# Performance work log

Hardware: AMD Instinct MI355X
Metric: run time of the kernel (lower is better)

## Reference

```python
import jax, jax.numpy as jnp
import numpy as np

B, D, H, N, M, K = 128, 256, 4, 256, 256, 10  # M=256 is hardcoded in the original repeat(1,1,1,256)
DIM = D // H  # per-head dim = 64


def setup_inputs() -> dict:
    key = jax.random.key(0)
    ks = jax.random.split(key, 10)
    s = 0.05  # weight scale
    return {
        "x": jax.random.normal(ks[0], (B, D, N), jnp.float32),
        "source": jax.random.normal(ks[1], (B, D, M), jnp.float32),
        "Wq": jax.random.normal(ks[2], (D, D), jnp.float32) * s,
        "bq": jax.random.normal(ks[3], (D,), jnp.float32) * s,
        "Wk": jax.random.normal(ks[4], (D, D), jnp.float32) * s,
        "bk": jax.random.normal(ks[5], (D,), jnp.float32) * s,
        "Wv": jax.random.normal(ks[6], (D, D), jnp.float32) * s,
        "bv": jax.random.normal(ks[7], (D,), jnp.float32) * s,
        "Wm": jax.random.normal(ks[8], (D, D), jnp.float32) * s,
        "bm": jax.random.normal(ks[9], (D,), jnp.float32) * s,
        "k": K,
    }


def _pointwise(W, b, x):
    # nn.Conv1d(d, d, kernel_size=1): per-point linear over channel dim
    return jnp.einsum('ef,bfn->ben', W, x) + b[None, :, None]


def reference(x, source, Wq, bq, Wk, bk, Wv, bv, Wm, bm, k):
    b, d, n = x.shape
    # torch .view(b, dim, heads, -1) splits channels as (dim, heads)
    q = _pointwise(Wq, bq, x).reshape(b, DIM, H, n)
    kk = _pointwise(Wk, bk, source).reshape(b, DIM, H, -1)
    v = _pointwise(Wv, bv, source).reshape(b, DIM, H, -1)

    scores = jnp.einsum('bdhn,bdhm->bhnm', q, kk) / jnp.sqrt(jnp.asarray(DIM, x.dtype))
    # per-row top-k threshold: keep only scores >= k-th largest, softmax over kept
    thresh = jax.lax.top_k(scores, k)[0][..., k - 1:k]  # [b,h,n,1]
    mask = scores >= thresh
    neg = jnp.finfo(scores.dtype).min
    prob = jax.nn.softmax(jnp.where(mask, scores, neg), axis=-1)
    prob = jnp.where(mask, prob, jnp.zeros((), scores.dtype))

    out = jnp.einsum('bhnm,bdhm->bdhn', prob, v).reshape(b, d, n)
    return _pointwise(Wm, bm, out)
```

## Files before the change

### kernel.cpp

```cpp
#include <hip/hip_runtime.h>
#include <hip/hip_bf16.h>

#define BB   128
#define DDIM 256
#define HH   4
#define NNN  256
#define MMM  256

typedef __hip_bfloat16 bf16;
typedef short  short8   __attribute__((ext_vector_type(8)));
typedef unsigned short ushort8_t __attribute__((ext_vector_type(8)));
typedef float  f32x4    __attribute__((ext_vector_type(4)));

__device__ __forceinline__ unsigned short f2bf(float x) {
    unsigned u = __builtin_bit_cast(unsigned, x);
    u += 0x7FFFu + ((u >> 16) & 1u);
    return (unsigned short)(u >> 16);
}
__device__ __forceinline__ float bf2f(unsigned short b) {
    unsigned u = ((unsigned)b) << 16;
    return __builtin_bit_cast(float, u);
}

__device__ __forceinline__ void xpose4(float v[4], const int p) {
    float ta = __shfl_xor((p & 1) ? v[0] : v[1], 1, 64);
    float tb = __shfl_xor((p & 1) ? v[2] : v[3], 1, 64);
    float u0 = (p & 1) ? ta : v[0];
    float u1 = (p & 1) ? v[1] : ta;
    float u2 = (p & 1) ? tb : v[2];
    float u3 = (p & 1) ? v[3] : tb;
    float tc = __shfl_xor((p & 2) ? u0 : u2, 2, 64);
    float td = __shfl_xor((p & 2) ? u1 : u3, 2, 64);
    v[0] = (p & 2) ? tc : u0;
    v[1] = (p & 2) ? td : u1;
    v[2] = (p & 2) ? u2 : tc;
    v[3] = (p & 2) ? u3 : td;
}

__device__ __forceinline__ void split3_store8k(char* dst, const float v[4]) {
    unsigned short h[4], m[4], l[4];
    #pragma unroll
    for (int i = 0; i < 4; ++i) {
        h[i] = f2bf(v[i]);
        float r1 = v[i] - bf2f(h[i]);
        m[i] = f2bf(r1);
        float r2 = r1 - bf2f(m[i]);
        l[i] = f2bf(r2);
    }
    uint2 hp, mp, lp;
    hp.x = (unsigned)h[0] | ((unsigned)h[1] << 16);
    hp.y = (unsigned)h[2] | ((unsigned)h[3] << 16);
    mp.x = (unsigned)m[0] | ((unsigned)m[1] << 16);
    mp.y = (unsigned)m[2] | ((unsigned)m[3] << 16);
    lp.x = (unsigned)l[0] | ((unsigned)l[1] << 16);
    lp.y = (unsigned)l[2] | ((unsigned)l[3] << 16);
    *(uint2*)dst = hp;
    *(uint2*)(dst + 8192) = mp;
    *(uint2*)(dst + 16384) = lp;
}

__device__ __forceinline__ void split2_store(char* dst, const float v[4]) {
    unsigned short h[4], m[4];
    #pragma unroll
    for (int i = 0; i < 4; ++i) {
        h[i] = f2bf(v[i]);
        float r1 = v[i] - bf2f(h[i]);
        m[i] = f2bf(r1);
    }
    uint2 hp, mp;
    hp.x = (unsigned)h[0] | ((unsigned)h[1] << 16);
    hp.y = (unsigned)h[2] | ((unsigned)h[3] << 16);
    mp.x = (unsigned)m[0] | ((unsigned)m[1] << 16);
    mp.y = (unsigned)m[2] | ((unsigned)m[3] << 16);
    *(uint2*)dst = hp;
    *(uint2*)(dst + 16384) = mp;
}

__device__ __forceinline__ void ldx4(const float* p, float v[4]) {
    const float4 f = *(const float4*)p;
    v[0] = f.x; v[1] = f.y; v[2] = f.z; v[3] = f.w;
}
__device__ __forceinline__ void ldx4(const bf16* p, float v[4]) {
    uint2 u = *(const uint2*)p;
    v[0] = bf2f((unsigned short)(u.x & 0xFFFF));
    v[1] = bf2f((unsigned short)(u.x >> 16));
    v[2] = bf2f((unsigned short)(u.y & 0xFFFF));
    v[3] = bf2f((unsigned short)(u.y >> 16));
}

__device__ __forceinline__ float max16v(const float* w) {
    float a = fmaxf(fmaxf(w[0], w[1]),  fmaxf(w[2], w[3]));
    float b = fmaxf(fmaxf(w[4], w[5]),  fmaxf(w[6], w[7]));
    float c = fmaxf(fmaxf(w[8], w[9]),  fmaxf(w[10], w[11]));
    float d = fmaxf(fmaxf(w[12], w[13]), fmaxf(w[14], w[15]));
    return fmaxf(fmaxf(a, b), fmaxf(c, d));
}
__device__ __forceinline__ float gmax16(float v) {
    v = fmaxf(v, __shfl_xor(v, 1, 64));
    v = fmaxf(v, __shfl_xor(v, 2, 64));
    v = fmaxf(v, __shfl_xor(v, 4, 64));
    v = fmaxf(v, __shfl_xor(v, 8, 64));
    return v;
}
__device__ __forceinline__ float gsum16(float v) {
    v += __shfl_xor(v, 1, 64);
    v += __shfl_xor(v, 2, 64);
    v += __shfl_xor(v, 4, 64);
    v += __shfl_xor(v, 8, 64);
    return v;
}

__global__ __launch_bounds__(256)
void proj_kernel(const float* __restrict__ X, const float* __restrict__ W,
                 const float* __restrict__ bias, float* __restrict__ Y) {
    __shared__ float Wt[32][68];
    __shared__ float Xt[32][132];

    const int t  = threadIdx.x;
    const int tx = t & 31;
    const int ty = t >> 5;
    const int n0 = blockIdx.x * 128;
    const int e0 = blockIdx.y * 64;
    const int b  = blockIdx.z;
    const size_t plane = (size_t)b * DDIM * NNN;

    float acc[8][4] = {};

    for (int f0 = 0; f0 < DDIM; f0 += 32) {
        #pragma unroll
        for (int i = 0; i < 8; ++i) {
            int idx = t + i * 256;
            int fl = idx & 31, el = idx >> 5;
            Wt[fl][el] = W[(size_t)(e0 + el) * DDIM + f0 + fl];
        }
        #pragma unroll
        for (int i = 0; i < 4; ++i) {
            int idx = t + i * 256;
            int fl = idx >> 5, nl4 = idx & 31;
            *(float4*)&Xt[fl][nl4 * 4] =
                *(const float4*)&X[plane + (size_t)(f0 + fl) * NNN + n0 + nl4 * 4];
        }
        __syncthreads();

        #pragma unroll
        for (int ff = 0; ff < 32; ++ff) {
            const float4 av0 = *(const float4*)&Wt[ff][ty * 8];
            const float4 av1 = *(const float4*)&Wt[ff][ty * 8 + 4];
            const float4 bv  = *(const float4*)&Xt[ff][tx * 4];
            const float a[8] = {av0.x, av0.y, av0.z, av0.w, av1.x, av1.y, av1.z, av1.w};
            const float c[4] = {bv.x, bv.y, bv.z, bv.w};
            #pragma unroll
            for (int i2 = 0; i2 < 8; ++i2)
                #pragma unroll
                for (int j = 0; j < 4; ++j)
                    acc[i2][j] = fmaf(a[i2], c[j], acc[i2][j]);
        }
        __syncthreads();
    }

    #pragma unroll
    for (int i2 = 0; i2 < 8; ++i2) {
        const int e = e0 + ty * 8 + i2;
        const float bs = bias[e];
        const size_t off = plane + (size_t)e * NNN + n0 + tx * 4;
        float4 o;
        o.x = acc[i2][0] + bs; o.y = acc[i2][1] + bs;
        o.z = acc[i2][2] + bs; o.w = acc[i2][3] + bs;
        *(float4*)&Y[off] = o;
    }
}

template <typename TIN, typename TOUT>
__global__ __launch_bounds__(512, 2)
void projm_kernel(const TIN* __restrict__ X, const float* __restrict__ W,
                  const float* __restrict__ bias, TOUT* __restrict__ Y) {
    extern __shared__ __align__(16) char smem[];

    const int t    = threadIdx.x;
    const int lane = t & 63;
    const int w    = t >> 6;
    const int c16  = lane & 15;
    const int g    = (lane >> 4) & 3;
    const int p    = lane & 3;
    const int G    = lane >> 2;

    const int n0 = blockIdx.x * 128;
    const int e0 = blockIdx.y * 128;
    const int b  = blockIdx.z;
    const size_t plane = (size_t)b * DDIM * NNN;

    f32x4 acc[8];
    #pragma unroll
    for (int nf = 0; nf < 8; ++nf) acc[nf] = f32x4{0.f, 0.f, 0.f, 0.f};

    #pragma unroll
    for (int ft = 0; ft < 4; ++ft) {
        const int f0 = ft * 64;
        if (ft) __syncthreads();
        #pragma unroll
        for (int it = 0; it < 4; ++it) {
            int chunk = w + 8 * it;
            int fch = chunk & 15, nh = chunk >> 4;
            float v[4];
            ldx4(&X[plane + (size_t)(f0 + fch * 4 + p) * NNN + n0 + nh * 64 + G * 4], v);
            xpose4(v, p);
            int nl = nh * 64 + G * 4 + p;
            int base = nl * 128 + ((fch * 8) ^ ((nl & 7) << 4));
            split2_store(smem + base, v);
        }
        #pragma unroll
        for (int it = 0; it < 4; ++it) {
            int idx = t + 512 * it;
            int el = idx >> 4, fq = idx & 15;
            float v[4];
            const float4 f4 = *(const float4*)&W[(size_t)(e0 + el) * DDIM + f0 + fq * 4];
            v[0] = f4.x; v[1] = f4.y; v[2] = f4.z; v[3] = f4.w;
            int base = 32768 + el * 128 + ((fq * 8) ^ ((el & 7) << 4));
            split2_store(smem + base, v);
        }
        __syncthreads();

        const int ew = w * 16;
        short8 a0[2], a1[2];
        #pragma unroll
        for (int ks = 0; ks < 2; ++ks) {
            int off = 32768 + (ew + c16) * 128
                    + ((ks * 64 + g * 16) ^ ((c16 & 7) << 4));
            a0[ks] = *(const short8*)(smem + off);
            a1[ks] = *(const short8*)(smem + off + 16384);
        }
        #pragma unroll
        for (int nf = 0; nf < 8; ++nf) {
            #pragma unroll
            for (int ks = 0; ks < 2; ++ks) {
                int off = (nf * 16 + c16) * 128
                        + ((ks * 64 + g * 16) ^ ((c16 & 7) << 4));
                short8 b0 = *(const short8*)(smem + off);
                short8 b1 = *(const short8*)(smem + off + 16384);
                f32x4 a = acc[nf];
                a = __builtin_amdgcn_mfma_f32_16x16x32_bf16(a0[ks], b0, a, 0, 0, 0);
                a = __builtin_amdgcn_mfma_f32_16x16x32_bf16(a0[ks], b1, a, 0, 0, 0);
                a = __builtin_amdgcn_mfma_f32_16x16x32_bf16(a1[ks], b0, a, 0, 0, 0);
                acc[nf] = a;
            }
        }
    }

    const int ew = w * 16;
    float bs[4];
    #pragma unroll
    for (int r = 0; r < 4; ++r) bs[r] = bias[e0 + ew + g * 4 + r];
    #pragma unroll
    for (int nf = 0; nf < 8; ++nf) {
        #pragma unroll
        for (int r = 0; r < 4; ++r) {
            size_t off = plane + (size_t)(e0 + ew + g * 4 + r) * NNN + n0 + nf * 16 + c16;
            float val = acc[nf][r] + bs[r];
            if constexpr (sizeof(TOUT) == 4) Y[off] = val;
            else                             *(unsigned short*)&Y[off] = f2bf(val);
        }
    }
}

__global__ __launch_bounds__(256, 3)
void attn3_kernel(const float* __restrict__ qf, const float* __restrict__ kf,
                  const bf16* __restrict__ vb, bf16* __restrict__ ob,
                  const int* __restrict__ kptr) {
    extern __shared__ __align__(16) char smem[];

    const int t    = threadIdx.x;
    const int lane = t & 63;
    const int w    = t >> 6;
    const int g    = lane >> 4;
    const int c16  = lane & 15;

    const int i    = blockIdx.x;
    const int work = (i & 7) * 256 + (i >> 3);
    const int bx = work & 3;
    const int h  = (work >> 2) & 3;
    const int b  = work >> 4;
    const int n0 = bx * 64;

    const size_t planeF = (size_t)b * DDIM * NNN;
    const size_t planeV = (size_t)b * DDIM * MMM;

    int kk = kptr[0];
    kk = kk < 1 ? 1 : (kk > MMM ? MMM : kk);

    {
        const int p = lane & 3, G = lane >> 2;
        #pragma unroll
        for (int it = 0; it < 4; ++it) {
            int dch = w + 4 * it;
            int drow = dch * 4 + p;
            float v[4];
            const float4 f4 = *(const float4*)&qf[planeF + (size_t)(drow * HH + h) * NNN + n0 + G * 4];
            v[0] = f4.x * 0.125f; v[1] = f4.y * 0.125f;
            v[2] = f4.z * 0.125f; v[3] = f4.w * 0.125f;
            xpose4(v, p);
            int nl = G * 4 + p;
            int base = nl * 128 + ((dch * 8) ^ ((nl & 7) << 4));
            split3_store8k(smem + base, v);
        }
    }
    __syncthreads();

    short8 qh[2], qm[2], ql[2];
    #pragma unroll
    for (int ks = 0; ks < 2; ++ks) {
        int nl = w * 16 + c16;
        int off = nl * 128 + ((ks * 64 + g * 16) ^ ((nl & 7) << 4));
        qh[ks] = *(const short8*)(smem + off);
        qm[ks] = *(const short8*)(smem + 8192 + off);
        ql[ks] = *(const short8*)(smem + 16384 + off);
    }

    f32x4 acc[16];
    #pragma unroll
    for (int m = 0; m < 16; ++m) acc[m] = f32x4{0.f, 0.f, 0.f, 0.f};

    #pragma unroll
    for (int tt = 0; tt < 4; ++tt) {
        if (tt) __syncthreads();
        {
            const int p = lane & 3, G = lane >> 2;
            #pragma unroll
            for (int it = 0; it < 4; ++it) {
                int dch = w + 4 * it;
                int drow = dch * 4 + p;
                int mcol = tt * 64 + G * 4;
                float v[4];
                const float4 f4 = *(const float4*)&kf[planeF + (size_t)(drow * HH + h) * MMM + mcol];
                v[0] = f4.x; v[1] = f4.y; v[2] = f4.z; v[3] = f4.w;
                xpose4(v, p);
                int ml = G * 4 + p;
                int base = 24576 + ml * 128 + ((dch * 8) ^ ((ml & 7) << 4));
                split3_store8k(smem + base, v);
            }
        }
        __syncthreads();
        #pragma unroll
        for (int mf = 0; mf < 4; ++mf) {
            #pragma unroll
            for (int ks = 0; ks < 2; ++ks) {
                int ml = mf * 16 + c16;
                int off = 24576 + ml * 128 + ((ks * 64 + g * 16) ^ ((ml & 7) << 4));
                short8 bh = *(const short8*)(smem + off);
                short8 bm = *(const short8*)(smem + 8192 + off);
                short8 bl = *(const short8*)(smem + 16384 + off);
                f32x4 a = acc[tt * 4 + mf];
                a = __builtin_amdgcn_mfma_f32_16x16x32_bf16(qh[ks], bh, a, 0, 0, 0);
                a = __builtin_amdgcn_mfma_f32_16x16x32_bf16(qh[ks], bm, a, 0, 0, 0);
                a = __builtin_amdgcn_mfma_f32_16x16x32_bf16(qm[ks], bh, a, 0, 0, 0);
                a = __builtin_amdgcn_mfma_f32_16x16x32_bf16(qm[ks], bm, a, 0, 0, 0);
                a = __builtin_amdgcn_mfma_f32_16x16x32_bf16(qh[ks], bl, a, 0, 0, 0);
                a = __builtin_amdgcn_mfma_f32_16x16x32_bf16(ql[ks], bh, a, 0, 0, 0);
                acc[tt * 4 + mf] = a;
            }
        }
    }
    __syncthreads();

    float thr[4], rmx[4];
    #pragma unroll
    for (int r = 0; r < 4; ++r) {
        float w16[16];
        #pragma unroll
        for (int mf = 0; mf < 16; ++mf) w16[mf] = acc[mf][r];
        float lm = max16v(w16);
        float gm = gmax16(lm);
        rmx[r] = gm;
        for (int it = 1; it < kk; ++it) {
            unsigned long long bal = __ballot(lm == gm);
            unsigned gmask = (unsigned)((bal >> (g * 16)) & 0xFFFFull);
            int leader = __builtin_ctz(gmask);
            bool skip = (c16 != leader);
            #pragma unroll
            for (int mf = 0; mf < 16; ++mf) {
                bool hit = (!skip) && (w16[mf] == gm);
                w16[mf] = hit ? -INFINITY : w16[mf];
                skip = skip || hit;
            }
            lm = max16v(w16);
            gm = gmax16(lm);
        }
        thr[r] = gm;
    }

    #pragma unroll
    for (int mf = 0; mf < 16; ++mf) {
        #pragma unroll
        for (int r = 0; r < 4; ++r) {
            float a = acc[mf][r];
            acc[mf][r] = (a >= thr[r]) ? __expf(a - rmx[r]) : 0.f;
        }
    }
    float inv_[4];
    #pragma unroll
    for (int r = 0; r < 4; ++r) {
        float s = ((acc[0][r] + acc[1][r]) + (acc[2][r] + acc[3][r]))
                + ((acc[4][r] + acc[5][r]) + (acc[6][r] + acc[7][r]))
                + ((acc[8][r] + acc[9][r]) + (acc[10][r] + acc[11][r]))
                + ((acc[12][r] + acc[13][r]) + (acc[14][r] + acc[15][r]));
        s = gsum16(s);
        inv_[r] = 1.0f / s;
    }
    #pragma unroll
    for (int mf = 0; mf < 16; ++mf) {
        #pragma unroll
        for (int r = 0; r < 4; ++r) {
            int row = w * 16 + g * 4 + r;
            int m2  = (mf * 16 + c16) * 2;
            int off = row * 512 + (m2 ^ ((row & 7) << 4));
            *(unsigned short*)(smem + off) = f2bf(acc[mf][r] * inv_[r]);
        }
    }

    f32x4 o[4];
    #pragma unroll
    for (int df = 0; df < 4; ++df) o[df] = f32x4{0.f, 0.f, 0.f, 0.f};

    #pragma unroll
    for (int half = 0; half < 2; ++half) {
        if (half) __syncthreads();
        #pragma unroll
        for (int it = 0; it < 4; ++it) {
            int idx = t + it * 256;
            int d = idx >> 4, mc8 = idx & 15;
            ushort8_t val = *(const ushort8_t*)
                &vb[planeV + (size_t)(d * HH + h) * MMM + half * 128 + mc8 * 8];
            int off = 32768 + d * 256 + ((mc8 * 16) ^ ((d & 7) << 4));
            *(ushort8_t*)(smem + off) = val;
        }
        __syncthreads();

        short8 pa[4];
        #pragma unroll
        for (int ks = 0; ks < 4; ++ks) {
            int row = w * 16 + c16;
            int off = row * 512 + ((half * 256 + ks * 64 + g * 16) ^ ((row & 7) << 4));
            pa[ks] = *(const short8*)(smem + off);
        }
        #pragma unroll
        for (int df = 0; df < 4; ++df) {
            int d = df * 16 + c16;
            f32x4 o_ = o[df];
            #pragma unroll
            for (int ks = 0; ks < 4; ++ks) {
                int off = 32768 + d * 256 + ((ks * 64 + g * 16) ^ ((d & 7) << 4));
                short8 vv = *(const short8*)(smem + off);
                o_ = __builtin_amdgcn_mfma_f32_16x16x32_bf16(pa[ks], vv, o_, 0, 0, 0);
            }
            o[df] = o_;
        }
    }
    __syncthreads();

    #pragma unroll
    for (int df = 0; df < 4; ++df)
        #pragma unroll
        for (int r = 0; r < 4; ++r) {
            int d  = df * 16 + c16;
            int nl = w * 16 + g * 4 + r;
            int off = d * 128 + ((nl * 2) ^ ((d & 7) << 4));
            *(unsigned short*)(smem + off) = f2bf(o[df][r]);
        }
    __syncthreads();
    #pragma unroll
    for (int it = 0; it < 2; ++it) {
        int idx = t + it * 256;
        int d = idx >> 3, ch = idx & 7;
        int off = d * 128 + ((ch * 16) ^ ((d & 7) << 4));
        ushort8_t val = *(const ushort8_t*)(smem + off);
        *(ushort8_t*)&ob[planeV + (size_t)(d * HH + h) * NNN + n0 + ch * 8] = val;
    }
}

extern "C" void kernel_launch(void* const* d_in, const int* in_sizes, int n_in,
                              void* d_out, int out_size, void* d_ws, size_t ws_size,
                              hipStream_t stream) {
    const float* x   = (const float*)d_in[0];
    const float* src = (const float*)d_in[1];
    const float* Wq  = (const float*)d_in[2];
    const float* bq  = (const float*)d_in[3];
    const float* Wk  = (const float*)d_in[4];
    const float* bk  = (const float*)d_in[5];
    const float* Wv  = (const float*)d_in[6];
    const float* bv  = (const float*)d_in[7];
    const float* Wm  = (const float*)d_in[8];
    const float* bm  = (const float*)d_in[9];
    const int*   kp  = (const int*)d_in[10];
    float* out = (float*)d_out;

    const size_t F32PLANE  = (size_t)BB * DDIM * NNN * sizeof(float);
    const size_t BF16PLANE = F32PLANE / 2;
    char* ws = (char*)d_ws;
    float* qf = (float*)(ws);
    float* kf = (float*)(ws + F32PLANE);
    bf16*  vb = (bf16*)(ws + 2 * F32PLANE);
    bf16*  ob = (bf16*)(ws + 2 * F32PLANE + BF16PLANE);

    hipFuncSetAttribute((const void*)(projm_kernel<float, bf16>),
                        hipFuncAttributeMaxDynamicSharedMemorySize, 65536);
    hipFuncSetAttribute((const void*)(projm_kernel<bf16, float>),
                        hipFuncAttributeMaxDynamicSharedMemorySize, 65536);
    hipFuncSetAttribute((const void*)attn3_kernel,
                        hipFuncAttributeMaxDynamicSharedMemorySize, 49152);

    dim3 fgrid(NNN / 128, DDIM / 64, BB);
    hipLaunchKernelGGL(proj_kernel, fgrid, dim3(256), 0, stream, x,   Wq, bq, qf);
    hipLaunchKernelGGL(proj_kernel, fgrid, dim3(256), 0, stream, src, Wk, bk, kf);

    dim3 mgrid(2, 2, BB);
    hipLaunchKernelGGL((projm_kernel<float, bf16>), mgrid, dim3(512), 65536, stream,
                       src, Wv, bv, vb);

    hipLaunchKernelGGL(attn3_kernel, dim3(2048), dim3(256), 49152, stream,
                       qf, kf, vb, ob, kp);

    hipLaunchKernelGGL((projm_kernel<bf16, float>), mgrid, dim3(512), 65536, stream,
                       ob, Wm, bm, out);
}
```

Measured before the change: 280.4 us.

## Cut attention LDS, sort-based top-k, direct V loads, packed FMA projections

Several changes land together. The attention kernel moves the K tile to offset zero and reuses the Q staging area, and it reads V straight from global memory instead of staging it in LDS. This drops its shared memory from 48KB to 32KB and raises the occupancy hint to 4 blocks. Top-k selection now sorts each lane's 16 scores once with a bitonic network and pops the head, replacing repeated max scans. The bf16-input output projection skips the redundant low-part split (fewer MFMAs, less LDS), and the fp32 projection uses packed 2-wide FMAs. Direct uncoalesced V loads from global memory could cost more than the LDS staging they replace.

```diff
diff --git a/kernel.cpp b/kernel.cpp
--- a/kernel.cpp
+++ b/kernel.cpp
@@ -11,6 +11,7 @@
 typedef short  short8   __attribute__((ext_vector_type(8)));
 typedef unsigned short ushort8_t __attribute__((ext_vector_type(8)));
 typedef float  f32x4    __attribute__((ext_vector_type(4)));
+typedef float  f32x2    __attribute__((ext_vector_type(2)));
 
 __device__ __forceinline__ unsigned short f2bf(float x) {
     unsigned u = __builtin_bit_cast(unsigned, x);
@@ -76,6 +77,13 @@
     *(uint2*)(dst + 16384) = mp;
 }
 
+__device__ __forceinline__ void split1_store(char* dst, const float v[4]) {
+    uint2 hp;
+    hp.x = (unsigned)f2bf(v[0]) | ((unsigned)f2bf(v[1]) << 16);
+    hp.y = (unsigned)f2bf(v[2]) | ((unsigned)f2bf(v[3]) << 16);
+    *(uint2*)dst = hp;
+}
+
 __device__ __forceinline__ void ldx4(const float* p, float v[4]) {
     const float4 f = *(const float4*)p;
     v[0] = f.x; v[1] = f.y; v[2] = f.z; v[3] = f.w;
@@ -88,13 +96,6 @@
     v[3] = bf2f((unsigned short)(u.y >> 16));
 }
 
-__device__ __forceinline__ float max16v(const float* w) {
-    float a = fmaxf(fmaxf(w[0], w[1]),  fmaxf(w[2], w[3]));
-    float b = fmaxf(fmaxf(w[4], w[5]),  fmaxf(w[6], w[7]));
-    float c = fmaxf(fmaxf(w[8], w[9]),  fmaxf(w[10], w[11]));
-    float d = fmaxf(fmaxf(w[12], w[13]), fmaxf(w[14], w[15]));
-    return fmaxf(fmaxf(a, b), fmaxf(c, d));
-}
 __device__ __forceinline__ float gmax16(float v) {
     v = fmaxf(v, __shfl_xor(v, 1, 64));
     v = fmaxf(v, __shfl_xor(v, 2, 64));
@@ -108,6 +109,26 @@
     v += __shfl_xor(v, 4, 64);
     v += __shfl_xor(v, 8, 64);
     return v;
+}
+
+__device__ __forceinline__ void sort16_desc(float w[16]) {
+    #pragma unroll
+    for (int k = 2; k <= 16; k <<= 1) {
+        #pragma unroll
+        for (int j = k >> 1; j > 0; j >>= 1) {
+            #pragma unroll
+            for (int i = 0; i < 16; ++i) {
+                const int l = i ^ j;
+                if (l > i) {
+                    const bool dmax = ((i & k) == 0);
+                    float mx = fmaxf(w[i], w[l]);
+                    float mn = fminf(w[i], w[l]);
+                    w[i] = dmax ? mx : mn;
+                    w[l] = dmax ? mn : mx;
+                }
+            }
+        }
+    }
 }
 
 __global__ __launch_bounds__(256)
@@ -124,7 +145,12 @@
     const int b  = blockIdx.z;
     const size_t plane = (size_t)b * DDIM * NNN;
 
-    float acc[8][4] = {};
+    f32x2 acc2[8][2];
+    #pragma unroll
+    for (int i = 0; i < 8; ++i) {
+        acc2[i][0] = f32x2{0.f, 0.f};
+        acc2[i][1] = f32x2{0.f, 0.f};
+    }
 
     for (int f0 = 0; f0 < DDIM; f0 += 32) {
         #pragma unroll
@@ -148,12 +174,14 @@
             const float4 av1 = *(const float4*)&Wt[ff][ty * 8 + 4];
             const float4 bv  = *(const float4*)&Xt[ff][tx * 4];
             const float a[8] = {av0.x, av0.y, av0.z, av0.w, av1.x, av1.y, av1.z, av1.w};
-            const float c[4] = {bv.x, bv.y, bv.z, bv.w};
-            #pragma unroll
-            for (int i2 = 0; i2 < 8; ++i2)
-                #pragma unroll
-                for (int j = 0; j < 4; ++j)
-                    acc[i2][j] = fmaf(a[i2], c[j], acc[i2][j]);
+            const f32x2 c0 = {bv.x, bv.y};
+            const f32x2 c1 = {bv.z, bv.w};
+            #pragma unroll
+            for (int i2 = 0; i2 < 8; ++i2) {
+                const f32x2 aa = {a[i2], a[i2]};
+                acc2[i2][0] = __builtin_elementwise_fma(aa, c0, acc2[i2][0]);
+                acc2[i2][1] = __builtin_elementwise_fma(aa, c1, acc2[i2][1]);
+            }
         }
         __syncthreads();
     }
@@ -164,106 +192,14 @@
         const float bs = bias[e];
         const size_t off = plane + (size_t)e * NNN + n0 + tx * 4;
         float4 o;
-        o.x = acc[i2][0] + bs; o.y = acc[i2][1] + bs;
-        o.z = acc[i2][2] + bs; o.w = acc[i2][3] + bs;
+        o.x = acc2[i2][0].x + bs; o.y = acc2[i2][0].y + bs;
+        o.z = acc2[i2][1].x + bs; o.w = acc2[i2][1].y + bs;
         *(float4*)&Y[off] = o;
     }
 }
 
-template <typename TIN, typename TOUT>
-__global__ __launch_bounds__(512, 2)
-void projm_kernel(const TIN* __restrict__ X, const float* __restrict__ W,
-                  const float* __restrict__ bias, TOUT* __restrict__ Y) {
-    extern __shared__ __align__(16) char smem[];
-
-    const int t    = threadIdx.x;
-    const int lane = t & 63;
-    const int w    = t >> 6;
-    const int c16  = lane & 15;
-    const int g    = (lane >> 4) & 3;
-    const int p    = lane & 3;
-    const int G    = lane >> 2;
-
-    const int n0 = blockIdx.x * 128;
-    const int e0 = blockIdx.y * 128;
-    const int b  = blockIdx.z;
-    const size_t plane = (size_t)b * DDIM * NNN;
-
-    f32x4 acc[8];
-    #pragma unroll
-    for (int nf = 0; nf < 8; ++nf) acc[nf] = f32x4{0.f, 0.f, 0.f, 0.f};
-
-    #pragma unroll
-    for (int ft = 0; ft < 4; ++ft) {
-        const int f0 = ft * 64;
-        if (ft) __syncthreads();
-        #pragma unroll
-        for (int it = 0; it < 4; ++it) {
-            int chunk = w + 8 * it;
-            int fch = chunk & 15, nh = chunk >> 4;
-            float v[4];
-            ldx4(&X[plane + (size_t)(f0 + fch * 4 + p) * NNN + n0 + nh * 64 + G * 4], v);
-            xpose4(v, p);
-            int nl = nh * 64 + G * 4 + p;
-            int base = nl * 128 + ((fch * 8) ^ ((nl & 7) << 4));
-            split2_store(smem + base, v);
-        }
-        #pragma unroll
-        for (int it = 0; it < 4; ++it) {
-            int idx = t + 512 * it;
-            int el = idx >> 4, fq = idx & 15;
-            float v[4];
-            const float4 f4 = *(const float4*)&W[(size_t)(e0 + el) * DDIM + f0 + fq * 4];
-            v[0] = f4.x; v[1] = f4.y; v[2] = f4.z; v[3] = f4.w;
-            int base = 32768 + el * 128 + ((fq * 8) ^ ((el & 7) << 4));
-            split2_store(smem + base, v);
-        }
-        __syncthreads();
-
-        const int ew = w * 16;
-        short8 a0[2], a1[2];
-        #pragma unroll
-        for (int ks = 0; ks < 2; ++ks) {
-            int off = 32768 + (ew + c16) * 128
-                    + ((ks * 64 + g * 16) ^ ((c16 & 7) << 4));
-            a0[ks] = *(const short8*)(smem + off);
-            a1[ks] = *(const short8*)(smem + off + 16384);
-        }
-        #pragma unroll
-        for (int nf = 0; nf < 8; ++nf) {
-            #pragma unroll
-            for (int ks = 0; ks < 2; ++ks) {
-                int off = (nf * 16 + c16) * 128
-                        + ((ks * 64 + g * 16) ^ ((c16 & 7) << 4));
-                short8 b0 = *(const short8*)(smem + off);
-                short8 b1 = *(const short8*)(smem + off + 16384);
-                f32x4 a = acc[nf];
-                a = __builtin_amdgcn_mfma_f32_16x16x32_bf16(a0[ks], b0, a, 0, 0, 0);
-                a = __builtin_amdgcn_mfma_f32_16x16x32_bf16(a0[ks], b1, a, 0, 0, 0);
-                a = __builtin_amdgcn_mfma_f32_16x16x32_bf16(a1[ks], b0, a, 0, 0, 0);
-                acc[nf] = a;
-            }
-        }
-    }
-
-    const int ew = w * 16;
-    float bs[4];
-    #pragma unroll
-    for (int r = 0; r < 4; ++r) bs[r] = bias[e0 + ew + g * 4 + r];
-    #pragma unroll
-    for (int nf = 0; nf < 8; ++nf) {
-        #pragma unroll
-        for (int r = 0; r < 4; ++r) {
-            size_t off = plane + (size_t)(e0 + ew + g * 4 + r) * NNN + n0 + nf * 16 + c16;
-            float val = acc[nf][r] + bs[r];
-            if constexpr (sizeof(TOUT) == 4) Y[off] = val;
-            else                             *(unsigned short*)&Y[off] = f2bf(val);
-        }
-    }
-}
-
-__global__ __launch_bounds__(256, 3)
-void attn3_kernel(const float* __restrict__ qf, const float* __restrict__ kf,
+__global__ __launch_bounds__(256, 4)
+void attn5_kernel(const float* __restrict__ qf, const float* __restrict__ kf,
                   const bf16* __restrict__ vb, bf16* __restrict__ ob,
                   const int* __restrict__ kptr) {
     extern __shared__ __align__(16) char smem[];
@@ -314,6 +250,7 @@
         qm[ks] = *(const short8*)(smem + 8192 + off);
         ql[ks] = *(const short8*)(smem + 16384 + off);
     }
+    __syncthreads();
 
     f32x4 acc[16];
     #pragma unroll
@@ -334,27 +271,28 @@
                 v[0] = f4.x; v[1] = f4.y; v[2] = f4.z; v[3] = f4.w;
                 xpose4(v, p);
                 int ml = G * 4 + p;
-                int base = 24576 + ml * 128 + ((dch * 8) ^ ((ml & 7) << 4));
+                int base = ml * 128 + ((dch * 8) ^ ((ml & 7) << 4));
                 split3_store8k(smem + base, v);
             }
         }
         __syncthreads();
+
         #pragma unroll
         for (int mf = 0; mf < 4; ++mf) {
             #pragma unroll
             for (int ks = 0; ks < 2; ++ks) {
                 int ml = mf * 16 + c16;
-                int off = 24576 + ml * 128 + ((ks * 64 + g * 16) ^ ((ml & 7) << 4));
-                short8 bh = *(const short8*)(smem + off);
-                short8 bm = *(const short8*)(smem + 8192 + off);
-                short8 bl = *(const short8*)(smem + 16384 + off);
+                int off = ml * 128 + ((ks * 64 + g * 16) ^ ((ml & 7) << 4));
+                short8 bh_ = *(const short8*)(smem + off);
+                short8 bm_ = *(const short8*)(smem + 8192 + off);
+                short8 bl_ = *(const short8*)(smem + 16384 + off);
                 f32x4 a = acc[tt * 4 + mf];
-                a = __builtin_amdgcn_mfma_f32_16x16x32_bf16(qh[ks], bh, a, 0, 0, 0);
-                a = __builtin_amdgcn_mfma_f32_16x16x32_bf16(qh[ks], bm, a, 0, 0, 0);
-                a = __builtin_amdgcn_mfma_f32_16x16x32_bf16(qm[ks], bh, a, 0, 0, 0);
-                a = __builtin_amdgcn_mfma_f32_16x16x32_bf16(qm[ks], bm, a, 0, 0, 0);
-                a = __builtin_amdgcn_mfma_f32_16x16x32_bf16(qh[ks], bl, a, 0, 0, 0);
-                a = __builtin_amdgcn_mfma_f32_16x16x32_bf16(ql[ks], bh, a, 0, 0, 0);
+                a = __builtin_amdgcn_mfma_f32_16x16x32_bf16(qh[ks], bh_, a, 0, 0, 0);
+                a = __builtin_amdgcn_mfma_f32_16x16x32_bf16(qh[ks], bm_, a, 0, 0, 0);
+                a = __builtin_amdgcn_mfma_f32_16x16x32_bf16(qm[ks], bh_, a, 0, 0, 0);
+                a = __builtin_amdgcn_mfma_f32_16x16x32_bf16(qm[ks], bm_, a, 0, 0, 0);
+                a = __builtin_amdgcn_mfma_f32_16x16x32_bf16(qh[ks], bl_, a, 0, 0, 0);
+                a = __builtin_amdgcn_mfma_f32_16x16x32_bf16(ql[ks], bh_, a, 0, 0, 0);
                 acc[tt * 4 + mf] = a;
             }
         }
@@ -364,25 +302,21 @@
     float thr[4], rmx[4];
     #pragma unroll
     for (int r = 0; r < 4; ++r) {
-        float w16[16];
-        #pragma unroll
-        for (int mf = 0; mf < 16; ++mf) w16[mf] = acc[mf][r];
-        float lm = max16v(w16);
-        float gm = gmax16(lm);
+        float s[16];
+        #pragma unroll
+        for (int mf = 0; mf < 16; ++mf) s[mf] = acc[mf][r];
+        sort16_desc(s);
+        float gm = gmax16(s[0]);
         rmx[r] = gm;
         for (int it = 1; it < kk; ++it) {
-            unsigned long long bal = __ballot(lm == gm);
+            unsigned long long bal = __ballot(s[0] == gm);
             unsigned gmask = (unsigned)((bal >> (g * 16)) & 0xFFFFull);
             int leader = __builtin_ctz(gmask);
-            bool skip = (c16 != leader);
-            #pragma unroll
-            for (int mf = 0; mf < 16; ++mf) {
-                bool hit = (!skip) && (w16[mf] == gm);
-                w16[mf] = hit ? -INFINITY : w16[mf];
-                skip = skip || hit;
-            }
-            lm = max16v(w16);
-            gm = gmax16(lm);
+            bool hit = (c16 == leader);
+            #pragma unroll
+            for (int j = 0; j < 15; ++j) s[j] = hit ? s[j + 1] : s[j];
+            s[15] = hit ? -INFINITY : s[15];
+            gm = gmax16(s[0]);
         }
         thr[r] = gm;
     }
@@ -415,6 +349,7 @@
             *(unsigned short*)(smem + off) = f2bf(acc[mf][r] * inv_[r]);
         }
     }
+    __syncthreads();
 
     f32x4 o[4];
     #pragma unroll
@@ -422,18 +357,6 @@
 
     #pragma unroll
     for (int half = 0; half < 2; ++half) {
-        if (half) __syncthreads();
-        #pragma unroll
-        for (int it = 0; it < 4; ++it) {
-            int idx = t + it * 256;
-            int d = idx >> 4, mc8 = idx & 15;
-            ushort8_t val = *(const ushort8_t*)
-                &vb[planeV + (size_t)(d * HH + h) * MMM + half * 128 + mc8 * 8];
-            int off = 32768 + d * 256 + ((mc8 * 16) ^ ((d & 7) << 4));
-            *(ushort8_t*)(smem + off) = val;
-        }
-        __syncthreads();
-
         short8 pa[4];
         #pragma unroll
         for (int ks = 0; ks < 4; ++ks) {
@@ -444,11 +367,11 @@
         #pragma unroll
         for (int df = 0; df < 4; ++df) {
             int d = df * 16 + c16;
+            const bf16* vrow = vb + planeV + (size_t)(d * HH + h) * MMM + half * 128;
             f32x4 o_ = o[df];
             #pragma unroll
             for (int ks = 0; ks < 4; ++ks) {
-                int off = 32768 + d * 256 + ((ks * 64 + g * 16) ^ ((d & 7) << 4));
-                short8 vv = *(const short8*)(smem + off);
+                short8 vv = *(const short8*)(vrow + ks * 32 + g * 8);
                 o_ = __builtin_amdgcn_mfma_f32_16x16x32_bf16(pa[ks], vv, o_, 0, 0, 0);
             }
             o[df] = o_;
@@ -473,6 +396,103 @@
         int off = d * 128 + ((ch * 16) ^ ((d & 7) << 4));
         ushort8_t val = *(const ushort8_t*)(smem + off);
         *(ushort8_t*)&ob[planeV + (size_t)(d * HH + h) * NNN + n0 + ch * 8] = val;
+    }
+}
+
+template <typename TIN, typename TOUT>
+__global__ __launch_bounds__(512, 2)
+void projm_kernel(const TIN* __restrict__ X, const float* __restrict__ W,
+                  const float* __restrict__ bias, TOUT* __restrict__ Y) {
+    extern __shared__ __align__(16) char smem[];
+    constexpr bool XBF = (sizeof(TIN) == 2);
+    constexpr int WOFF = XBF ? 16384 : 32768;
+
+    const int t    = threadIdx.x;
+    const int lane = t & 63;
+    const int w    = t >> 6;
+    const int c16  = lane & 15;
+    const int g    = (lane >> 4) & 3;
+    const int p    = lane & 3;
+    const int G    = lane >> 2;
+
+    const int n0 = blockIdx.x * 128;
+    const int e0 = blockIdx.y * 128;
+    const int b  = blockIdx.z;
+    const size_t plane = (size_t)b * DDIM * NNN;
+
+    f32x4 acc[8];
+    #pragma unroll
+    for (int nf = 0; nf < 8; ++nf) acc[nf] = f32x4{0.f, 0.f, 0.f, 0.f};
+
+    #pragma unroll
+    for (int ft = 0; ft < 4; ++ft) {
+        const int f0 = ft * 64;
+        if (ft) __syncthreads();
+        #pragma unroll
+        for (int it = 0; it < 4; ++it) {
+            int chunk = w + 8 * it;
+            int fch = chunk & 15, nh = chunk >> 4;
+            float v[4];
+            ldx4(&X[plane + (size_t)(f0 + fch * 4 + p) * NNN + n0 + nh * 64 + G * 4], v);
+            xpose4(v, p);
+            int nl = nh * 64 + G * 4 + p;
+            int base = nl * 128 + ((fch * 8) ^ ((nl & 7) << 4));
+            if constexpr (XBF) split1_store(smem + base, v);
+            else               split2_store(smem + base, v);
+        }
+        #pragma unroll
+        for (int it = 0; it < 4; ++it) {
+            int idx = t + 512 * it;
+            int el = idx >> 4, fq = idx & 15;
+            float v[4];
+            const float4 f4 = *(const float4*)&W[(size_t)(e0 + el) * DDIM + f0 + fq * 4];
+            v[0] = f4.x; v[1] = f4.y; v[2] = f4.z; v[3] = f4.w;
+            int base = WOFF + el * 128 + ((fq * 8) ^ ((el & 7) << 4));
+            split2_store(smem + base, v);
+        }
+        __syncthreads();
+
+        const int ew = w * 16;
+        short8 a0[2], a1[2];
+        #pragma unroll
+        for (int ks = 0; ks < 2; ++ks) {
+            int off = WOFF + (ew + c16) * 128
+                    + ((ks * 64 + g * 16) ^ ((c16 & 7) << 4));
+            a0[ks] = *(const short8*)(smem + off);
+            a1[ks] = *(const short8*)(smem + off + 16384);
+        }
+        #pragma unroll
+        for (int nf = 0; nf < 8; ++nf) {
+            #pragma unroll
+            for (int ks = 0; ks < 2; ++ks) {
+                int off = (nf * 16 + c16) * 128
+                        + ((ks * 64 + g * 16) ^ ((c16 & 7) << 4));
+                short8 b0 = *(const short8*)(smem + off);
+                f32x4 a = acc[nf];
+                a = __builtin_amdgcn_mfma_f32_16x16x32_bf16(a0[ks], b0, a, 0, 0, 0);
+                if constexpr (!XBF) {
+                    short8 b1 = *(const short8*)(smem + off + 16384);
+                    a = __builtin_amdgcn_mfma_f32_16x16x32_bf16(a0[ks], b1, a, 0, 0, 0);
+                }
+                a = __builtin_amdgcn_mfma_f32_16x16x32_bf16(a1[ks], b0, a, 0, 0, 0);
+                acc[nf] = a;
+            }
+        }
+    }
+
+    const int ew = w * 16;
+    float bs[4];
+    #pragma unroll
+    for (int r = 0; r < 4; ++r) bs[r] = bias[e0 + ew + g * 4 + r];
+    #pragma unroll
+    for (int nf = 0; nf < 8; ++nf) {
+        #pragma unroll
+        for (int r = 0; r < 4; ++r) {
+            size_t off = plane + (size_t)(e0 + ew + g * 4 + r) * NNN + n0 + nf * 16 + c16;
+            float val = acc[nf][r] + bs[r];
+            if constexpr (sizeof(TOUT) == 4) Y[off] = val;
+            else                             *(unsigned short*)&Y[off] = f2bf(val);
+        }
     }
 }
 
@@ -492,9 +512,10 @@
     const int*   kp  = (const int*)d_in[10];
     float* out = (float*)d_out;
 
-    const size_t F32PLANE  = (size_t)BB * DDIM * NNN * sizeof(float);
-    const size_t BF16PLANE = F32PLANE / 2;
     char* ws = (char*)d_ws;
+    const size_t F32PLANE  = 33554432;
+    const size_t BF16PLANE = 16777216;
+
     float* qf = (float*)(ws);
     float* kf = (float*)(ws + F32PLANE);
     bf16*  vb = (bf16*)(ws + 2 * F32PLANE);
@@ -503,21 +524,21 @@
     hipFuncSetAttribute((const void*)(projm_kernel<float, bf16>),
                         hipFuncAttributeMaxDynamicSharedMemorySize, 65536);
     hipFuncSetAttribute((const void*)(projm_kernel<bf16, float>),
-                        hipFuncAttributeMaxDynamicSharedMemorySize, 65536);
-    hipFuncSetAttribute((const void*)attn3_kernel,
                         hipFuncAttributeMaxDynamicSharedMemorySize, 49152);
-
-    dim3 fgrid(NNN / 128, DDIM / 64, BB);
-    hipLaunchKernelGGL(proj_kernel, fgrid, dim3(256), 0, stream, x,   Wq, bq, qf);
-    hipLaunchKernelGGL(proj_kernel, fgrid, dim3(256), 0, stream, src, Wk, bk, kf);
-
+    hipFuncSetAttribute((const void*)attn5_kernel,
+                        hipFuncAttributeMaxDynamicSharedMemorySize, 32768);
+
+    dim3 pgrid(NNN / 128, DDIM / 64, BB);
     dim3 mgrid(2, 2, BB);
+
+    hipLaunchKernelGGL(proj_kernel, pgrid, dim3(256), 0, stream,
+                       x,   Wq, bq, qf);
+    hipLaunchKernelGGL(proj_kernel, pgrid, dim3(256), 0, stream,
+                       src, Wk, bk, kf);
     hipLaunchKernelGGL((projm_kernel<float, bf16>), mgrid, dim3(512), 65536, stream,
                        src, Wv, bv, vb);
-
-    hipLaunchKernelGGL(attn3_kernel, dim3(2048), dim3(256), 49152, stream,
+    hipLaunchKernelGGL(attn5_kernel, dim3(2048), dim3(256), 32768, stream,
                        qf, kf, vb, ob, kp);
-
-    hipLaunchKernelGGL((projm_kernel<bf16, float>), mgrid, dim3(512), 65536, stream,
+    hipLaunchKernelGGL((projm_kernel<bf16, float>), mgrid, dim3(512), 49152, stream,
                        ob, Wm, bm, out);
 }
```

After: 249.2 us. -11.1%, faster.
